# Performance work log

Hardware: AMD Instinct MI355X
Metric: run time of the kernel (lower is better)

Reference implementation:

```python
import jax, jax.numpy as jnp
import numpy as np

SMOOTH = 1e-05
N_SCALES = 3
# 3x3 cross-shaped boundary kernel, OIHW layout [1,1,3,3]
_KERNEL = jnp.array([[0., 1., 0.], [1., 1., 1.], [0., 1., 0.]], jnp.float32).reshape(1, 1, 3, 3)


def _nearest_ds(t, h, w):
    """torch F.interpolate mode='nearest': src_idx = floor(dst_idx * in/out)."""
    H, W = t.shape[-2], t.shape[-1]
    ih = (jnp.arange(h) * H) // h
    iw = (jnp.arange(w) * W) // w
    return t[..., ih[:, None], iw[None, :]]


def _boundary_dou(probs, tgt, valid):
    # probs, tgt: [B,N,h,w] float32; valid: [B,N] float32 in {0,1}
    B, N, h, w = probs.shape
    Y = jax.lax.conv_general_dilated(
        tgt.reshape(B * N, 1, h, w), _KERNEL,
        window_strides=(1, 1), padding=[(1, 1), (1, 1)],
        dimension_numbers=('NCHW', 'OIHW', 'NCHW')).reshape(B, N, h, w)
    Y = Y * tgt
    Y = jnp.where(Y == 5.0, 0.0, Y)  # interior pixels zeroed, boundary kept
    C = jnp.sum(Y != 0, axis=(-2, -1)).astype(jnp.float32)   # [B,N] boundary count
    S = jnp.sum(tgt != 0, axis=(-2, -1)).astype(jnp.float32)  # [B,N] fg count
    alpha = 2.0 * (1.0 - (C + SMOOTH) / (S + SMOOTH)) - 1.0
    alpha = jnp.minimum(alpha, 0.8)
    inter = jnp.sum(probs * tgt, axis=(-2, -1))
    y_sum = jnp.sum(tgt * tgt, axis=(-2, -1))
    z_sum = jnp.sum(probs * probs, axis=(-2, -1))
    dou = (z_sum + y_sum - 2.0 * inter + SMOOTH) / (z_sum + y_sum - (1.0 + alpha) * inter + SMOOTH)
    per = jnp.where(S > 0, dou, probs.mean(axis=(-2, -1)))  # empty-target fallback
    cnt = valid.sum()
    return jnp.where(cnt > 0, (per * valid).sum() / cnt, 0.0)


def reference(logits0, logits1, logits2, targets, valid_mask):
    outs = [logits0, logits1, logits2]
    ws = np.array([1.0 / 2.0 ** i for i in range(N_SCALES)])
    ws = ws / ws.sum()  # nnU-Net deep supervision weights
    tgt_full = targets.astype(jnp.float32)
    valid = (valid_mask >= 0.5).astype(jnp.float32)
    loss = jnp.float32(0.0)
    for w_i, out in zip(ws, outs):
        h, w = out.shape[-2], out.shape[-1]
        tgt = _nearest_ds(tgt_full, h, w)
        probs = jax.nn.sigmoid(out.astype(jnp.float32))
        loss = loss + jnp.float32(w_i) * _boundary_dou(probs, tgt, valid)
    return loss


def setup_inputs() -> dict:
    key = jax.random.key(0)
    k0, k1, k2, kt = jax.random.split(key, 4)
    B, N = 8, 4
    return {
        'logits0': jax.random.normal(k0, (B, N, 512, 512), jnp.float32),
        'logits1': jax.random.normal(k1, (B, N, 256, 256), jnp.float32),
        'logits2': jax.random.normal(k2, (B, N, 128, 128), jnp.float32),
        'targets': jax.random.randint(kt, (B, N, 512, 512), 0, 2, jnp.int32),
        'valid_mask': jnp.ones((B, N), jnp.float32),
    }
```

## Files before the change

### kernel.cpp

```cpp
#include <hip/hip_runtime.h>

#define SMOOTH 1e-5f

typedef float floatx4 __attribute__((ext_vector_type(4)));
typedef float floatx2 __attribute__((ext_vector_type(2)));


__device__ __forceinline__ float wave_reduce(float v) {
#pragma unroll
    for (int off = 32; off; off >>= 1) v += __shfl_down(v, off, 64);
    return v;
}

__device__ __forceinline__ float sigmoidf(float x) {
    return 1.f / (1.f + __expf(-x));
}

__device__ __forceinline__ unsigned pack8(int4 a, int4 b) {
    return (unsigned)(a.x != 0)        | ((unsigned)(a.y != 0) << 1) |
           ((unsigned)(a.z != 0) << 2) | ((unsigned)(a.w != 0) << 3) |
           ((unsigned)(b.x != 0) << 4) | ((unsigned)(b.y != 0) << 5) |
           ((unsigned)(b.z != 0) << 6) | ((unsigned)(b.w != 0) << 7);
}
__device__ __forceinline__ unsigned pack4(int4 a, int4 b) {
    return (unsigned)(a.x != 0)        | ((unsigned)(a.z != 0) << 1) |
           ((unsigned)(b.x != 0) << 2) | ((unsigned)(b.z != 0) << 3);
}
__device__ __forceinline__ unsigned pack2(int a, int b) {
    return (unsigned)(a != 0) | ((unsigned)(b != 0) << 1);
}

template<int W>
__device__ __forceinline__ void row_proc(unsigned u, unsigned c, unsigned d,
    const float* pr, int lane, int& cC, int& cS, float& aI, float& aZ, float& aP)
{
    unsigned pv = __shfl_up(c, 1);
    unsigned nx = __shfl_down(c, 1);
    if (lane == 0)  pv = 0;
    if (lane == 63) nx = 0;
    const unsigned M = (1u << W) - 1u;
    unsigned lv = ((c << 1) | ((pv >> (W - 1)) & 1u)) & M;
    unsigned rv = ((c >> 1) | ((nx & 1u) << (W - 1))) & M;
    unsigned inter = c & u & d & lv & rv;
    cS += __popc(c);
    cC += __popc(c & ~inter);
#pragma unroll
    for (int j = 0; j < W; ++j) {
        float pj = pr[j];
        aI += ((c >> j) & 1u) ? pj : 0.f;
        aZ += pj * pj;
        aP += pj;
    }
}

__global__ __launch_bounds__(256) void bdou_reduce(
    const float* __restrict__ l0, const float* __restrict__ l1,
    const float* __restrict__ l2, const int* __restrict__ tgt,
    float* __restrict__ ws)
{
    const int blk = blockIdx.x;
    const int tid = threadIdx.x;
    const int w   = tid >> 6, lane = tid & 63;

    int scale, img, rb;
    if (blk < 1024)      { scale = 0; img = blk >> 5; rb = blk & 31; }
    else if (blk < 1536) { int b = blk - 1024; scale = 1; img = b >> 4; rb = b & 15; }
    else                 { int b = blk - 1536; scale = 2; img = b >> 3; rb = b & 7; }

    const int* __restrict__ timg = tgt + (size_t)img * 262144;
    const int y0 = rb * 16 + w * 4;

    int   cC = 0, cS = 0;
    float aI = 0.f, aZ = 0.f, aP = 0.f;

    if (scale == 0) {
        const int cc = lane * 8;
        const int* T = timg + (size_t)y0 * 512 + cc;
        const float* L = l0 + (size_t)img * 262144 + (size_t)y0 * 512 + cc;
        const int ou = (y0 > 0) ? -512 : 0;
        const unsigned mu = (y0 > 0) ? 0xFFu : 0u;
        const int od = (y0 + 4 <= 511) ? 4 * 512 : 3 * 512;
        const unsigned m4 = (y0 + 4 <= 511) ? 0xFFu : 0u;
        int4 ru0 = *(const int4*)(T + ou),       ru1 = *(const int4*)(T + ou + 4);
        int4 r00 = *(const int4*)(T),            r01 = *(const int4*)(T + 4);
        int4 r10 = *(const int4*)(T + 512),      r11 = *(const int4*)(T + 512 + 4);
        int4 r20 = *(const int4*)(T + 1024),     r21 = *(const int4*)(T + 1024 + 4);
        int4 r30 = *(const int4*)(T + 1536),     r31 = *(const int4*)(T + 1536 + 4);
        int4 r40 = *(const int4*)(T + od),       r41 = *(const int4*)(T + od + 4);
        floatx4 la0 = *(const floatx4*)(L),              la1 = *(const floatx4*)(L + 4);
        floatx4 lb0 = *(const floatx4*)(L + 512),        lb1 = *(const floatx4*)(L + 512 + 4);
        floatx4 lc0 = *(const floatx4*)(L + 1024),       lc1 = *(const floatx4*)(L + 1024 + 4);
        floatx4 ld0 = *(const floatx4*)(L + 1536),       ld1 = *(const floatx4*)(L + 1536 + 4);
        unsigned bu = pack8(ru0, ru1) & mu;
        unsigned b0 = pack8(r00, r01);
        unsigned b1 = pack8(r10, r11);
        unsigned b2 = pack8(r20, r21);
        unsigned b3 = pack8(r30, r31);
        unsigned b4 = pack8(r40, r41) & m4;
        float pr[8];
        pr[0]=sigmoidf(la0.x); pr[1]=sigmoidf(la0.y); pr[2]=sigmoidf(la0.z); pr[3]=sigmoidf(la0.w);
        pr[4]=sigmoidf(la1.x); pr[5]=sigmoidf(la1.y); pr[6]=sigmoidf(la1.z); pr[7]=sigmoidf(la1.w);
        row_proc<8>(bu, b0, b1, pr, lane, cC, cS, aI, aZ, aP);
        pr[0]=sigmoidf(lb0.x); pr[1]=sigmoidf(lb0.y); pr[2]=sigmoidf(lb0.z); pr[3]=sigmoidf(lb0.w);
        pr[4]=sigmoidf(lb1.x); pr[5]=sigmoidf(lb1.y); pr[6]=sigmoidf(lb1.z); pr[7]=sigmoidf(lb1.w);
        row_proc<8>(b0, b1, b2, pr, lane, cC, cS, aI, aZ, aP);
        pr[0]=sigmoidf(lc0.x); pr[1]=sigmoidf(lc0.y); pr[2]=sigmoidf(lc0.z); pr[3]=sigmoidf(lc0.w);
        pr[4]=sigmoidf(lc1.x); pr[5]=sigmoidf(lc1.y); pr[6]=sigmoidf(lc1.z); pr[7]=sigmoidf(lc1.w);
        row_proc<8>(b1, b2, b3, pr, lane, cC, cS, aI, aZ, aP);
        pr[0]=sigmoidf(ld0.x); pr[1]=sigmoidf(ld0.y); pr[2]=sigmoidf(ld0.z); pr[3]=sigmoidf(ld0.w);
        pr[4]=sigmoidf(ld1.x); pr[5]=sigmoidf(ld1.y); pr[6]=sigmoidf(ld1.z); pr[7]=sigmoidf(ld1.w);
        row_proc<8>(b2, b3, b4, pr, lane, cC, cS, aI, aZ, aP);
    } else if (scale == 1) {
        const int fc = lane * 8;
        const int* T = timg + (size_t)(2 * y0) * 512 + fc;
        const float* L = l1 + (size_t)img * 65536 + (size_t)y0 * 256 + lane * 4;
        const int ou = (y0 > 0) ? -1024 : 0;
        const unsigned mu = (y0 > 0) ? 0xFu : 0u;
        const int od = (y0 + 4 <= 255) ? 4096 : 3072;
        const unsigned m4 = (y0 + 4 <= 255) ? 0xFu : 0u;
        int4 ru0 = *(const int4*)(T + ou),   ru1 = *(const int4*)(T + ou + 4);
        int4 r00 = *(const int4*)(T),        r01 = *(const int4*)(T + 4);
        int4 r10 = *(const int4*)(T + 1024), r11 = *(const int4*)(T + 1024 + 4);
        int4 r20 = *(const int4*)(T + 2048), r21 = *(const int4*)(T + 2048 + 4);
        int4 r30 = *(const int4*)(T + 3072), r31 = *(const int4*)(T + 3072 + 4);
        int4 r40 = *(const int4*)(T + od),   r41 = *(const int4*)(T + od + 4);
        floatx4 la = *(const floatx4*)(L);
        floatx4 lb = *(const floatx4*)(L + 256);
        floatx4 lc = *(const floatx4*)(L + 512);
        floatx4 ld = *(const floatx4*)(L + 768);
        unsigned bu = pack4(ru0, ru1) & mu;
        unsigned b0 = pack4(r00, r01);
        unsigned b1 = pack4(r10, r11);
        unsigned b2 = pack4(r20, r21);
        unsigned b3 = pack4(r30, r31);
        unsigned b4 = pack4(r40, r41) & m4;
        float pr[4];
        pr[0]=sigmoidf(la.x); pr[1]=sigmoidf(la.y); pr[2]=sigmoidf(la.z); pr[3]=sigmoidf(la.w);
        row_proc<4>(bu, b0, b1, pr, lane, cC, cS, aI, aZ, aP);
        pr[0]=sigmoidf(lb.x); pr[1]=sigmoidf(lb.y); pr[2]=sigmoidf(lb.z); pr[3]=sigmoidf(lb.w);
        row_proc<4>(b0, b1, b2, pr, lane, cC, cS, aI, aZ, aP);
        pr[0]=sigmoidf(lc.x); pr[1]=sigmoidf(lc.y); pr[2]=sigmoidf(lc.z); pr[3]=sigmoidf(lc.w);
        row_proc<4>(b1, b2, b3, pr, lane, cC, cS, aI, aZ, aP);
        pr[0]=sigmoidf(ld.x); pr[1]=sigmoidf(ld.y); pr[2]=sigmoidf(ld.z); pr[3]=sigmoidf(ld.w);
        row_proc<4>(b2, b3, b4, pr, lane, cC, cS, aI, aZ, aP);
    } else {
        const int fc = lane * 8;
        const int* T = timg + (size_t)(4 * y0) * 512 + fc;
        const float* L = l2 + (size_t)img * 16384 + (size_t)y0 * 128 + lane * 2;
        const int ou = (y0 > 0) ? -2048 : 0;
        const unsigned mu = (y0 > 0) ? 3u : 0u;
        const int od = (y0 + 4 <= 127) ? 8192 : 6144;
        const unsigned m4 = (y0 + 4 <= 127) ? 3u : 0u;
        int ru0 = T[ou],   ru1 = T[ou + 4];
        int r00 = T[0],    r01 = T[4];
        int r10 = T[2048], r11 = T[2048 + 4];
        int r20 = T[4096], r21 = T[4096 + 4];
        int r30 = T[6144], r31 = T[6144 + 4];
        int r40 = T[od],   r41 = T[od + 4];
        floatx2 la = *(const floatx2*)(L);
        floatx2 lb = *(const floatx2*)(L + 128);
        floatx2 lc = *(const floatx2*)(L + 256);
        floatx2 ld = *(const floatx2*)(L + 384);
        unsigned bu = pack2(ru0, ru1) & mu;
        unsigned b0 = pack2(r00, r01);
        unsigned b1 = pack2(r10, r11);
        unsigned b2 = pack2(r20, r21);
        unsigned b3 = pack2(r30, r31);
        unsigned b4 = pack2(r40, r41) & m4;
        float pr[2];
        pr[0]=sigmoidf(la.x); pr[1]=sigmoidf(la.y);
        row_proc<2>(bu, b0, b1, pr, lane, cC, cS, aI, aZ, aP);
        pr[0]=sigmoidf(lb.x); pr[1]=sigmoidf(lb.y);
        row_proc<2>(b0, b1, b2, pr, lane, cC, cS, aI, aZ, aP);
        pr[0]=sigmoidf(lc.x); pr[1]=sigmoidf(lc.y);
        row_proc<2>(b1, b2, b3, pr, lane, cC, cS, aI, aZ, aP);
        pr[0]=sigmoidf(ld.x); pr[1]=sigmoidf(ld.y);
        row_proc<2>(b2, b3, b4, pr, lane, cC, cS, aI, aZ, aP);
    }

    float vals[5] = {(float)cC, (float)cS, aI, aZ, aP};
    __shared__ float red[4][5];
#pragma unroll
    for (int k = 0; k < 5; ++k) vals[k] = wave_reduce(vals[k]);
    if (lane == 0) {
#pragma unroll
        for (int k = 0; k < 5; ++k) red[w][k] = vals[k];
    }
    __syncthreads();
    if (tid < 5) {
        float s = red[0][tid] + red[1][tid] + red[2][tid] + red[3][tid];
        atomicAdd(&ws[(scale * 32 + img) * 5 + tid], s);
    }
}

__global__ void bdou_final(const float* __restrict__ ws,
                           const float* __restrict__ valid_mask,
                           float* __restrict__ out)
{
    int tid = threadIdx.x;
    float contrib = 0.f, cpart = 0.f;
    if (tid < 96) {
        int s = tid >> 5, i = tid & 31;
        const float* w = ws + tid * 5;
        float C = w[0], S = w[1], I = w[2], Z = w[3], P = w[4];
        float valid = (valid_mask[i] >= 0.5f) ? 1.f : 0.f;
        float alpha = fminf(2.f * (1.f - (C + SMOOTH) / (S + SMOOTH)) - 1.f, 0.8f);
        float dou = (Z + S - 2.f * I + SMOOTH) /
                    (Z + S - (1.f + alpha) * I + SMOOTH);
        const float wts[3]  = {4.f / 7.f, 2.f / 7.f, 1.f / 7.f};
        const float pixc[3] = {262144.f, 65536.f, 16384.f};
        float per = (S > 0.f) ? dou : (P / pixc[s]);
        contrib = wts[s] * per * valid;
        if (tid < 32) cpart = valid;
    }
    contrib = wave_reduce(contrib);
    cpart   = wave_reduce(cpart);
    __shared__ float sm[2][2];
    int wv = tid >> 6, ln = tid & 63;
    if (ln == 0) { sm[wv][0] = contrib; sm[wv][1] = cpart; }
    __syncthreads();
    if (tid == 0) {
        float tot = sm[0][0] + sm[1][0];
        float cnt = sm[0][1] + sm[1][1];
        out[0] = (cnt > 0.f) ? tot / cnt : 0.f;
    }
}

extern "C" void kernel_launch(void* const* d_in, const int* in_sizes, int n_in,
                              void* d_out, int out_size, void* d_ws, size_t ws_size,
                              hipStream_t stream) {
    const float* l0 = (const float*)d_in[0];
    const float* l1 = (const float*)d_in[1];
    const float* l2 = (const float*)d_in[2];
    const int*   tg = (const int*)d_in[3];
    const float* vm = (const float*)d_in[4];
    float* ws = (float*)d_ws;

    (void)hipMemsetAsync(ws, 0, 3 * 32 * 5 * sizeof(float), stream);
    bdou_reduce<<<1792, 256, 0, stream>>>(l0, l1, l2, tg, ws);
    bdou_final<<<1, 128, 0, stream>>>(ws, vm, (float*)d_out);
}
```

Baseline: 113.1 us.

## Stream 16-row strips per single wave with rolling target bitmasks

Each block is now a single 64-lane wave that walks 16 consecutive rows. It keeps previous, current and next packed target rows in registers and prefetches the next row's target and logits, instead of four waves each reloading a 6-row halo for 4 rows. This cuts redundant halo reads of the target tensor and removes the shared-memory reduction and barrier, with lane 0 issuing the atomics directly. In exchange there are far fewer threads in flight (1792 x 64), which may reduce memory-level parallelism for a bandwidth-bound kernel.

```diff
diff --git a/kernel.cpp b/kernel.cpp
--- a/kernel.cpp
+++ b/kernel.cpp
@@ -53,143 +53,127 @@
     }
 }
 
-__global__ __launch_bounds__(256) void bdou_reduce(
+__global__ __launch_bounds__(64) void bdou_reduce(
     const float* __restrict__ l0, const float* __restrict__ l1,
     const float* __restrict__ l2, const int* __restrict__ tgt,
     float* __restrict__ ws)
 {
-    const int blk = blockIdx.x;
-    const int tid = threadIdx.x;
-    const int w   = tid >> 6, lane = tid & 63;
-
-    int scale, img, rb;
-    if (blk < 1024)      { scale = 0; img = blk >> 5; rb = blk & 31; }
-    else if (blk < 1536) { int b = blk - 1024; scale = 1; img = b >> 4; rb = b & 15; }
-    else                 { int b = blk - 1536; scale = 2; img = b >> 3; rb = b & 7; }
+    const int blk  = blockIdx.x;
+    const int lane = threadIdx.x;
+
+    int scale, img, strip;
+    if (blk < 1024)      { scale = 0; img = blk >> 5; strip = blk & 31; }
+    else if (blk < 1536) { int b = blk - 1024; scale = 1; img = b >> 4; strip = b & 15; }
+    else                 { int b = blk - 1536; scale = 2; img = b >> 3; strip = b & 7; }
 
     const int* __restrict__ timg = tgt + (size_t)img * 262144;
-    const int y0 = rb * 16 + w * 4;
+    const int y0 = strip * 16;
 
     int   cC = 0, cS = 0;
     float aI = 0.f, aZ = 0.f, aP = 0.f;
 
     if (scale == 0) {
-        const int cc = lane * 8;
-        const int* T = timg + (size_t)y0 * 512 + cc;
-        const float* L = l0 + (size_t)img * 262144 + (size_t)y0 * 512 + cc;
-        const int ou = (y0 > 0) ? -512 : 0;
-        const unsigned mu = (y0 > 0) ? 0xFFu : 0u;
-        const int od = (y0 + 4 <= 511) ? 4 * 512 : 3 * 512;
-        const unsigned m4 = (y0 + 4 <= 511) ? 0xFFu : 0u;
-        int4 ru0 = *(const int4*)(T + ou),       ru1 = *(const int4*)(T + ou + 4);
-        int4 r00 = *(const int4*)(T),            r01 = *(const int4*)(T + 4);
-        int4 r10 = *(const int4*)(T + 512),      r11 = *(const int4*)(T + 512 + 4);
-        int4 r20 = *(const int4*)(T + 1024),     r21 = *(const int4*)(T + 1024 + 4);
-        int4 r30 = *(const int4*)(T + 1536),     r31 = *(const int4*)(T + 1536 + 4);
-        int4 r40 = *(const int4*)(T + od),       r41 = *(const int4*)(T + od + 4);
-        floatx4 la0 = *(const floatx4*)(L),              la1 = *(const floatx4*)(L + 4);
-        floatx4 lb0 = *(const floatx4*)(L + 512),        lb1 = *(const floatx4*)(L + 512 + 4);
-        floatx4 lc0 = *(const floatx4*)(L + 1024),       lc1 = *(const floatx4*)(L + 1024 + 4);
-        floatx4 ld0 = *(const floatx4*)(L + 1536),       ld1 = *(const floatx4*)(L + 1536 + 4);
-        unsigned bu = pack8(ru0, ru1) & mu;
-        unsigned b0 = pack8(r00, r01);
-        unsigned b1 = pack8(r10, r11);
-        unsigned b2 = pack8(r20, r21);
-        unsigned b3 = pack8(r30, r31);
-        unsigned b4 = pack8(r40, r41) & m4;
-        float pr[8];
-        pr[0]=sigmoidf(la0.x); pr[1]=sigmoidf(la0.y); pr[2]=sigmoidf(la0.z); pr[3]=sigmoidf(la0.w);
-        pr[4]=sigmoidf(la1.x); pr[5]=sigmoidf(la1.y); pr[6]=sigmoidf(la1.z); pr[7]=sigmoidf(la1.w);
-        row_proc<8>(bu, b0, b1, pr, lane, cC, cS, aI, aZ, aP);
-        pr[0]=sigmoidf(lb0.x); pr[1]=sigmoidf(lb0.y); pr[2]=sigmoidf(lb0.z); pr[3]=sigmoidf(lb0.w);
-        pr[4]=sigmoidf(lb1.x); pr[5]=sigmoidf(lb1.y); pr[6]=sigmoidf(lb1.z); pr[7]=sigmoidf(lb1.w);
-        row_proc<8>(b0, b1, b2, pr, lane, cC, cS, aI, aZ, aP);
-        pr[0]=sigmoidf(lc0.x); pr[1]=sigmoidf(lc0.y); pr[2]=sigmoidf(lc0.z); pr[3]=sigmoidf(lc0.w);
-        pr[4]=sigmoidf(lc1.x); pr[5]=sigmoidf(lc1.y); pr[6]=sigmoidf(lc1.z); pr[7]=sigmoidf(lc1.w);
-        row_proc<8>(b1, b2, b3, pr, lane, cC, cS, aI, aZ, aP);
-        pr[0]=sigmoidf(ld0.x); pr[1]=sigmoidf(ld0.y); pr[2]=sigmoidf(ld0.z); pr[3]=sigmoidf(ld0.w);
-        pr[4]=sigmoidf(ld1.x); pr[5]=sigmoidf(ld1.y); pr[6]=sigmoidf(ld1.z); pr[7]=sigmoidf(ld1.w);
-        row_proc<8>(b2, b3, b4, pr, lane, cC, cS, aI, aZ, aP);
+        const int*   T = timg + lane * 8;
+        const float* L = l0 + (size_t)img * 262144 + lane * 8;
+        unsigned b_prev, b_cur, b_next;
+        floatx4 lgA, lgB;
+        {
+            int yp = (y0 > 0) ? y0 - 1 : 0;
+            int4 a0 = *(const int4*)(T + (size_t)yp * 512);
+            int4 a1 = *(const int4*)(T + (size_t)yp * 512 + 4);
+            int4 c0 = *(const int4*)(T + (size_t)y0 * 512);
+            int4 c1 = *(const int4*)(T + (size_t)y0 * 512 + 4);
+            int4 d0 = *(const int4*)(T + (size_t)(y0 + 1) * 512);
+            int4 d1 = *(const int4*)(T + (size_t)(y0 + 1) * 512 + 4);
+            lgA = *(const floatx4*)(L + (size_t)y0 * 512);
+            lgB = *(const floatx4*)(L + (size_t)y0 * 512 + 4);
+            b_prev = pack8(a0, a1); b_cur = pack8(c0, c1); b_next = pack8(d0, d1);
+        }
+        for (int i = 0; i < 16; ++i) {
+            int y   = y0 + i;
+            int ypf = (y + 2 < 512) ? y + 2 : 511;
+            int ylg = (y + 1 < 512) ? y + 1 : 511;
+            int4 p0 = *(const int4*)(T + (size_t)ypf * 512);
+            int4 p1 = *(const int4*)(T + (size_t)ypf * 512 + 4);
+            floatx4 nA = *(const floatx4*)(L + (size_t)ylg * 512);
+            floatx4 nB = *(const floatx4*)(L + (size_t)ylg * 512 + 4);
+            unsigned u = (y > 0)   ? b_prev : 0u;
+            unsigned d = (y < 511) ? b_next : 0u;
+            float pr[8] = {sigmoidf(lgA.x), sigmoidf(lgA.y), sigmoidf(lgA.z), sigmoidf(lgA.w),
+                           sigmoidf(lgB.x), sigmoidf(lgB.y), sigmoidf(lgB.z), sigmoidf(lgB.w)};
+            row_proc<8>(u, b_cur, d, pr, lane, cC, cS, aI, aZ, aP);
+            b_prev = b_cur; b_cur = b_next; b_next = pack8(p0, p1);
+            lgA = nA; lgB = nB;
+        }
     } else if (scale == 1) {
-        const int fc = lane * 8;
-        const int* T = timg + (size_t)(2 * y0) * 512 + fc;
-        const float* L = l1 + (size_t)img * 65536 + (size_t)y0 * 256 + lane * 4;
-        const int ou = (y0 > 0) ? -1024 : 0;
-        const unsigned mu = (y0 > 0) ? 0xFu : 0u;
-        const int od = (y0 + 4 <= 255) ? 4096 : 3072;
-        const unsigned m4 = (y0 + 4 <= 255) ? 0xFu : 0u;
-        int4 ru0 = *(const int4*)(T + ou),   ru1 = *(const int4*)(T + ou + 4);
-        int4 r00 = *(const int4*)(T),        r01 = *(const int4*)(T + 4);
-        int4 r10 = *(const int4*)(T + 1024), r11 = *(const int4*)(T + 1024 + 4);
-        int4 r20 = *(const int4*)(T + 2048), r21 = *(const int4*)(T + 2048 + 4);
-        int4 r30 = *(const int4*)(T + 3072), r31 = *(const int4*)(T + 3072 + 4);
-        int4 r40 = *(const int4*)(T + od),   r41 = *(const int4*)(T + od + 4);
-        floatx4 la = *(const floatx4*)(L);
-        floatx4 lb = *(const floatx4*)(L + 256);
-        floatx4 lc = *(const floatx4*)(L + 512);
-        floatx4 ld = *(const floatx4*)(L + 768);
-        unsigned bu = pack4(ru0, ru1) & mu;
-        unsigned b0 = pack4(r00, r01);
-        unsigned b1 = pack4(r10, r11);
-        unsigned b2 = pack4(r20, r21);
-        unsigned b3 = pack4(r30, r31);
-        unsigned b4 = pack4(r40, r41) & m4;
-        float pr[4];
-        pr[0]=sigmoidf(la.x); pr[1]=sigmoidf(la.y); pr[2]=sigmoidf(la.z); pr[3]=sigmoidf(la.w);
-        row_proc<4>(bu, b0, b1, pr, lane, cC, cS, aI, aZ, aP);
-        pr[0]=sigmoidf(lb.x); pr[1]=sigmoidf(lb.y); pr[2]=sigmoidf(lb.z); pr[3]=sigmoidf(lb.w);
-        row_proc<4>(b0, b1, b2, pr, lane, cC, cS, aI, aZ, aP);
-        pr[0]=sigmoidf(lc.x); pr[1]=sigmoidf(lc.y); pr[2]=sigmoidf(lc.z); pr[3]=sigmoidf(lc.w);
-        row_proc<4>(b1, b2, b3, pr, lane, cC, cS, aI, aZ, aP);
-        pr[0]=sigmoidf(ld.x); pr[1]=sigmoidf(ld.y); pr[2]=sigmoidf(ld.z); pr[3]=sigmoidf(ld.w);
-        row_proc<4>(b2, b3, b4, pr, lane, cC, cS, aI, aZ, aP);
+        const int*   T = timg + lane * 8;
+        const float* L = l1 + (size_t)img * 65536 + lane * 4;
+        unsigned b_prev, b_cur, b_next;
+        floatx4 lgA;
+        {
+            int yp = (y0 > 0) ? y0 - 1 : 0;
+            int4 a0 = *(const int4*)(T + (size_t)(2 * yp) * 512);
+            int4 a1 = *(const int4*)(T + (size_t)(2 * yp) * 512 + 4);
+            int4 c0 = *(const int4*)(T + (size_t)(2 * y0) * 512);
+            int4 c1 = *(const int4*)(T + (size_t)(2 * y0) * 512 + 4);
+            int4 d0 = *(const int4*)(T + (size_t)(2 * (y0 + 1)) * 512);
+            int4 d1 = *(const int4*)(T + (size_t)(2 * (y0 + 1)) * 512 + 4);
+            lgA = *(const floatx4*)(L + (size_t)y0 * 256);
+            b_prev = pack4(a0, a1); b_cur = pack4(c0, c1); b_next = pack4(d0, d1);
+        }
+        for (int i = 0; i < 16; ++i) {
+            int y   = y0 + i;
+            int ypf = (y + 2 < 256) ? y + 2 : 255;
+            int ylg = (y + 1 < 256) ? y + 1 : 255;
+            int4 p0 = *(const int4*)(T + (size_t)(2 * ypf) * 512);
+            int4 p1 = *(const int4*)(T + (size_t)(2 * ypf) * 512 + 4);
+            floatx4 nA = *(const floatx4*)(L + (size_t)ylg * 256);
+            unsigned u = (y > 0)   ? b_prev : 0u;
+            unsigned d = (y < 255) ? b_next : 0u;
+            float pr[4] = {sigmoidf(lgA.x), sigmoidf(lgA.y), sigmoidf(lgA.z), sigmoidf(lgA.w)};
+            row_proc<4>(u, b_cur, d, pr, lane, cC, cS, aI, aZ, aP);
+            b_prev = b_cur; b_cur = b_next; b_next = pack4(p0, p1);
+            lgA = nA;
+        }
     } else {
-        const int fc = lane * 8;
-        const int* T = timg + (size_t)(4 * y0) * 512 + fc;
-        const float* L = l2 + (size_t)img * 16384 + (size_t)y0 * 128 + lane * 2;
-        const int ou = (y0 > 0) ? -2048 : 0;
-        const unsigned mu = (y0 > 0) ? 3u : 0u;
-        const int od = (y0 + 4 <= 127) ? 8192 : 6144;
-        const unsigned m4 = (y0 + 4 <= 127) ? 3u : 0u;
-        int ru0 = T[ou],   ru1 = T[ou + 4];
-        int r00 = T[0],    r01 = T[4];
-        int r10 = T[2048], r11 = T[2048 + 4];
-        int r20 = T[4096], r21 = T[4096 + 4];
-        int r30 = T[6144], r31 = T[6144 + 4];
-        int r40 = T[od],   r41 = T[od + 4];
-        floatx2 la = *(const floatx2*)(L);
-        floatx2 lb = *(const floatx2*)(L + 128);
-        floatx2 lc = *(const floatx2*)(L + 256);
-        floatx2 ld = *(const floatx2*)(L + 384);
-        unsigned bu = pack2(ru0, ru1) & mu;
-        unsigned b0 = pack2(r00, r01);
-        unsigned b1 = pack2(r10, r11);
-        unsigned b2 = pack2(r20, r21);
-        unsigned b3 = pack2(r30, r31);
-        unsigned b4 = pack2(r40, r41) & m4;
-        float pr[2];
-        pr[0]=sigmoidf(la.x); pr[1]=sigmoidf(la.y);
-        row_proc<2>(bu, b0, b1, pr, lane, cC, cS, aI, aZ, aP);
-        pr[0]=sigmoidf(lb.x); pr[1]=sigmoidf(lb.y);
-        row_proc<2>(b0, b1, b2, pr, lane, cC, cS, aI, aZ, aP);
-        pr[0]=sigmoidf(lc.x); pr[1]=sigmoidf(lc.y);
-        row_proc<2>(b1, b2, b3, pr, lane, cC, cS, aI, aZ, aP);
-        pr[0]=sigmoidf(ld.x); pr[1]=sigmoidf(ld.y);
-        row_proc<2>(b2, b3, b4, pr, lane, cC, cS, aI, aZ, aP);
+        const int*   T = timg + lane * 8;
+        const float* L = l2 + (size_t)img * 16384 + lane * 2;
+        unsigned b_prev, b_cur, b_next;
+        floatx2 lgA;
+        {
+            int yp = (y0 > 0) ? y0 - 1 : 0;
+            int a0 = T[(size_t)(4 * yp) * 512],       a1 = T[(size_t)(4 * yp) * 512 + 4];
+            int c0 = T[(size_t)(4 * y0) * 512],       c1 = T[(size_t)(4 * y0) * 512 + 4];
+            int d0 = T[(size_t)(4 * (y0 + 1)) * 512], d1 = T[(size_t)(4 * (y0 + 1)) * 512 + 4];
+            lgA = *(const floatx2*)(L + (size_t)y0 * 128);
+            b_prev = pack2(a0, a1); b_cur = pack2(c0, c1); b_next = pack2(d0, d1);
+        }
+        for (int i = 0; i < 16; ++i) {
+            int y   = y0 + i;
+            int ypf = (y + 2 < 128) ? y + 2 : 127;
+            int ylg = (y + 1 < 128) ? y + 1 : 127;
+            int p0 = T[(size_t)(4 * ypf) * 512];
+            int p1 = T[(size_t)(4 * ypf) * 512 + 4];
+            floatx2 nA = *(const floatx2*)(L + (size_t)ylg * 128);
+            unsigned u = (y > 0)   ? b_prev : 0u;
+            unsigned d = (y < 127) ? b_next : 0u;
+            float pr[2] = {sigmoidf(lgA.x), sigmoidf(lgA.y)};
+            row_proc<2>(u, b_cur, d, pr, lane, cC, cS, aI, aZ, aP);
+            b_prev = b_cur; b_cur = b_next; b_next = pack2(p0, p1);
+            lgA = nA;
+        }
     }
 
     float vals[5] = {(float)cC, (float)cS, aI, aZ, aP};
-    __shared__ float red[4][5];
 #pragma unroll
     for (int k = 0; k < 5; ++k) vals[k] = wave_reduce(vals[k]);
     if (lane == 0) {
-#pragma unroll
-        for (int k = 0; k < 5; ++k) red[w][k] = vals[k];
-    }
-    __syncthreads();
-    if (tid < 5) {
-        float s = red[0][tid] + red[1][tid] + red[2][tid] + red[3][tid];
-        atomicAdd(&ws[(scale * 32 + img) * 5 + tid], s);
+        float* w = ws + (scale * 32 + img) * 5;
+        atomicAdd(&w[0], vals[0]);
+        atomicAdd(&w[1], vals[1]);
+        atomicAdd(&w[2], vals[2]);
+        atomicAdd(&w[3], vals[3]);
+        atomicAdd(&w[4], vals[4]);
     }
 }
 
@@ -237,6 +221,6 @@
     float* ws = (float*)d_ws;
 
     (void)hipMemsetAsync(ws, 0, 3 * 32 * 5 * sizeof(float), stream);
-    bdou_reduce<<<1792, 256, 0, stream>>>(l0, l1, l2, tg, ws);
+    bdou_reduce<<<1792, 64, 0, stream>>>(l0, l1, l2, tg, ws);
     bdou_final<<<1, 128, 0, stream>>>(ws, vm, (float*)d_out);
 }
```

Measured after the change: 125.6 us. 1.11x slower.
